# Kernel tuning notes

Measured on AMD Instinct MI355X. Metric: run time of the kernel, lower is better.

## Reference

```python
import jax, jax.numpy as jnp
import numpy as np

S, B, H, D, G = 2048, 2, 16, 128, 16  # seq, batch, heads, head_dim, v-quant groups


def setup_inputs() -> dict:
    key = jax.random.key(0)
    ks = jax.random.split(key, 9)
    # int8-valued activations stored as float (torch code does .to(torch.int8))
    q = jax.random.randint(ks[0], (S, B, H, D), -128, 128).astype(jnp.float32)
    k = jax.random.randint(ks[1], (S, B, H, D), -128, 128).astype(jnp.float32)
    v = jax.random.randint(ks[2], (S, B, H, D), -128, 128).astype(jnp.float32)
    qmin = jax.random.normal(ks[3], (S, B, H, 1), jnp.float32) * 0.01
    qscale = jax.random.uniform(ks[4], (S, B, H, 1), jnp.float32, 0.005, 0.02)
    kmin = jax.random.normal(ks[5], (S, B, H, 1), jnp.float32) * 0.01
    kscale = jax.random.uniform(ks[6], (S, B, H, 1), jnp.float32, 0.005, 0.02)
    vmin = jax.random.normal(ks[7], (G, B, H, D, 1), jnp.float32) * 0.01
    vscale = jax.random.uniform(ks[8], (G, B, H, D, 1), jnp.float32, 0.005, 0.02)
    return {"query_layer": q, "key_layer": k, "value_layer": v,
            "qmin": qmin, "qscale": qscale, "kmin": kmin, "kscale": kscale,
            "vmin": vmin, "vscale": vscale, "causal": 1}


def _attention(query_layer, key_layer, value_layer, qmin, qscale, kmin, kscale, vmin, vscale, causal):
    # s b h d -> b h s d ; emulate .to(torch.int8) (values are already int8-range ints)
    q = jnp.transpose(query_layer, (1, 2, 0, 3))
    k = jnp.transpose(key_layer, (1, 2, 0, 3))
    v = jnp.transpose(value_layer, (1, 2, 0, 3))
    # per-token quant factors: s b h 1 -> b h s 1
    qm = jnp.transpose(qmin[..., 0], (1, 2, 0))[..., None]
    qs = jnp.transpose(qscale[..., 0], (1, 2, 0))[..., None]
    km = jnp.transpose(kmin[..., 0], (1, 2, 0))[..., None]
    ksc = jnp.transpose(kscale[..., 0], (1, 2, 0))[..., None]
    # attnq_qk: dequantize per-token then QK^T
    qd = q * qs + qm
    kd = k * ksc + km
    scores = jnp.einsum('bhsd,bhtd->bhst', qd, kd)
    # softmaxq: scale by 1/sqrt(128), causal mask, softmax, int8 requant of probs
    scores = scores * jnp.float32(1.0 / np.sqrt(128.0))
    s = scores.shape[-1]
    if causal:
        mask = jnp.tril(jnp.ones((s, s), dtype=bool))
        scores = jnp.where(mask, scores, jnp.float32(-1e9))
    probs = jax.nn.softmax(scores, axis=-1)
    pmin = jnp.min(probs, axis=-1, keepdims=True)
    pmax = jnp.max(probs, axis=-1, keepdims=True)
    pscale = (pmax - pmin) / 255.0 + jnp.float32(1e-12)
    quant_prob = jnp.round((probs - pmin) / pscale)  # int8-range prob codes
    # attnq_pv: dequant probs (per query token) and V (per sequence group) then PV
    pd = quant_prob * pscale + pmin
    vm = jnp.transpose(vmin[..., 0], (1, 2, 0, 3))  # b h g d
    vs = jnp.transpose(vscale[..., 0], (1, 2, 0, 3))
    gs = v.shape[2] // vm.shape[2]  # group size along sequence
    vd = v * jnp.repeat(vs, gs, axis=2) + jnp.repeat(vm, gs, axis=2)
    out = jnp.einsum('bhst,bhtd->bhsd', pd, vd)
    b, h, sq, d = out.shape
    return jnp.transpose(out, (2, 0, 1, 3)).reshape(sq, b, h * d)  # s b (h d)


def reference(query_layer, key_layer, value_layer, qmin, qscale, kmin, kscale, vmin, vscale, causal):
    return _attention(query_layer, key_layer, value_layer, qmin, qscale, kmin, kscale, vmin, vscale, causal)
```

## Files before the change

### kernel.cpp

```cpp
#include <hip/hip_runtime.h>
#include <math.h>


#define S_LEN 2048
#define BATCH 2
#define NH    16
#define HD    128
#define RSTR  4096
#define SCALE2 (0.08838834764831845f * 1.4426950408889634f)
#define EXP2F(x) __builtin_amdgcn_exp2f(x)

typedef int v4i __attribute__((ext_vector_type(4)));
#define MFMA16(a,b,c) __builtin_amdgcn_mfma_i32_16x16x64_i8((a),(b),(c),0,0,0)

#define WS_K8   0u
#define WS_V8T  (8u*1024u*1024u)
#define WS_SQ   (16u*1024u*1024u)
#define WS_SK   (WS_SQ + 256u*1024u)
#define WS_GSV  (WS_SK + 256u*1024u)

__device__ __forceinline__ int sbsum(unsigned p) {
    return (int)(signed char)(p) + (int)(signed char)(p>>8)
         + (int)(signed char)(p>>16) + (int)(signed char)(p>>24);
}

__global__ __launch_bounds__(256) void prep_pack(
    const float* __restrict__ Q, const float* __restrict__ K, const float* __restrict__ V,
    signed char* __restrict__ K8, float* __restrict__ SQs, float* __restrict__ SKs,
    signed char* __restrict__ V8T, float* __restrict__ GSV)
{
    __shared__ int v8i[128*33];
    const int tid = threadIdx.x;
    const int bx  = blockIdx.x;
    if (bx < 16384) {
        const int tensor = bx >> 13;
        const int idx = (bx & 8191)*256 + tid;
        const float* src = tensor ? K : Q;
        int tau = idx >> 5, dg = idx & 31;
        float4 x = *(const float4*)(src + (size_t)tau*128 + 4*dg);
        float ssum = x.x + x.y + x.z + x.w;
        #pragma unroll
        for (int off = 16; off >= 1; off >>= 1) ssum += __shfl_xor(ssum, off);
        if (tensor) {
            int a=(int)x.x, b2=(int)x.y, c=(int)x.z, d=(int)x.w;
            ((int*)K8)[(size_t)tau*32 + dg] = (a&255)|((b2&255)<<8)|((c&255)<<16)|((d&255)<<24);
            if ((tid & 31) == 0) SKs[tau] = ssum;
        } else {
            if ((tid & 31) == 0) SQs[tau] = ssum;
        }
    } else {
        const int bid = bx - 16384;
        const int bh = bid & 31, ck = bid >> 5;
        const int b = bh >> 4, h = bh & 15;
        const int t0 = ck * 128;
        const int boff = b*2048 + h*128;
        #pragma unroll
        for (int it = 0; it < 16; ++it) {
            int idx = tid + it*256;
            int t = idx >> 5, dw = idx & 31;
            float4 x = *(const float4*)(V + (size_t)(t0+t)*RSTR + boff + 4*dw);
            int a=(int)x.x, b2=(int)x.y, c=(int)x.z, d=(int)x.w;
            v8i[t*33 + dw] = (a&255)|((b2&255)<<8)|((c&255)<<16)|((d&255)<<24);
        }
        __syncthreads();
        #pragma unroll
        for (int it = 0; it < 4; ++it) {
            int j = tid + it*256;
            int tg = j & 31, dw = j >> 5;
            unsigned r0 = (unsigned)v8i[(4*tg+0)*33 + dw];
            unsigned r1 = (unsigned)v8i[(4*tg+1)*33 + dw];
            unsigned r2 = (unsigned)v8i[(4*tg+2)*33 + dw];
            unsigned r3 = (unsigned)v8i[(4*tg+3)*33 + dw];
            unsigned x01 = __builtin_amdgcn_perm(r1, r0, 0x05010400u);
            unsigned x23 = __builtin_amdgcn_perm(r3, r2, 0x05010400u);
            unsigned y01 = __builtin_amdgcn_perm(r1, r0, 0x07030602u);
            unsigned y23 = __builtin_amdgcn_perm(r3, r2, 0x07030602u);
            unsigned p[4];
            p[0] = __builtin_amdgcn_perm(x23, x01, 0x05040100u);
            p[1] = __builtin_amdgcn_perm(x23, x01, 0x07060302u);
            p[2] = __builtin_amdgcn_perm(y23, y01, 0x05040100u);
            p[3] = __builtin_amdgcn_perm(y23, y01, 0x07060302u);
            int s[4];
            #pragma unroll
            for (int jj = 0; jj < 4; ++jj) {
                int d = 4*dw + jj;
                *(int*)(V8T + ((size_t)bh*128 + d)*2048 + t0 + 4*tg) = (int)p[jj];
                s[jj] = sbsum(p[jj]);
            }
            #pragma unroll
            for (int off = 1; off < 32; off <<= 1) {
                #pragma unroll
                for (int jj = 0; jj < 4; ++jj) s[jj] += __shfl_xor(s[jj], off);
            }
            if (tg == 0) {
                #pragma unroll
                for (int jj = 0; jj < 4; ++jj)
                    GSV[((size_t)bh*16 + ck)*128 + 4*dw + jj] = (float)s[jj];
            }
        }
    }
}

__global__ __launch_bounds__(256, 2) void attn_main(
    const float* __restrict__ Q,
    const signed char* __restrict__ K8, const signed char* __restrict__ V8T,
    const float* __restrict__ QMN, const float* __restrict__ QSC,
    const float* __restrict__ KMN, const float* __restrict__ KSC,
    const float* __restrict__ VMN, const float* __restrict__ VSC,
    const float* __restrict__ SQs, const float* __restrict__ SKs,
    const float* __restrict__ GSV,
    const int* __restrict__ CAUSAL, float* __restrict__ OUT)
{
    __shared__ __align__(16) signed char q8s[64*144];
    __shared__ __align__(16) signed char k8s[128*144];
    __shared__ __align__(16) signed char v8s[128*144];
    __shared__ __align__(16) signed char pcs[64*144];
    __shared__ float rs_c1[64], rs_c2[64], rs_c3[64];
    __shared__ float rs_mx[64], rs_den[64], rs_mn[64];
    __shared__ float rs_u1[64], rs_w1[64], rs_psc[64], rs_pmn[64];
    __shared__ float ktA[128], ktB[128], ktC[128];
    __shared__ float vsA[128], vsB[128];
    __shared__ float vsumL[128], cgsL[128];

    const int tid  = threadIdx.x;
    const int w    = tid >> 6;
    const int lane = tid & 63;
    const int n    = lane & 15;
    const int quad = lane >> 4;
    const int bhi  = blockIdx.x & 31;
    const int qt   = 31 - (int)(blockIdx.x >> 5);
    const int b    = bhi >> 4, h = bhi & 15;
    const int causal = *CAUSAL;
    const int s0   = qt * 64;
    const int boff = b*2048 + h*128;
    const v4i vzero = {0,0,0,0};
    const v4i ones  = {0x01010101,0x01010101,0x01010101,0x01010101};

    #pragma unroll
    for (int it = 0; it < 8; ++it) {
        int idx = tid + it*256;
        int row = idx >> 5, d4 = (idx & 31) << 2;
        float4 x = *(const float4*)(Q + (size_t)(s0+row)*RSTR + boff + d4);
        int a=(int)x.x, b2=(int)x.y, c=(int)x.z, d=(int)x.w;
        *(int*)(q8s + row*144 + d4) = (a&255)|((b2&255)<<8)|((c&255)<<16)|((d&255)<<24);
    }
    if (tid < 64) {
        int si = (s0 + tid)*32 + bhi;
        float qs = QSC[si], qm = QMN[si];
        rs_c1[tid] = qs; rs_c2[tid] = qm;
        rs_c3[tid] = fmaf(qs, SQs[si], 128.0f*qm);
    }
    __syncthreads();

    const int kt_end = causal ? ((s0 + 63) >> 7) : 15;

    float c1r[4], c2r[4], c3r[4]; int qgr[4];
    #pragma unroll
    for (int r = 0; r < 4; ++r) {
        int qq = 16*w + 4*quad + r;
        c1r[r] = rs_c1[qq]; c2r[r] = rs_c2[qq]; c3r[r] = rs_c3[qq];
        qgr[r] = s0 + qq;
    }
    v4i a0p = *(const v4i*)(q8s + (16*w + n)*144 + 16*quad);
    v4i a1p = *(const v4i*)(q8s + (16*w + n)*144 + 64 + 16*quad);

    float m[4], l[4], mn[4];
    #pragma unroll
    for (int r = 0; r < 4; ++r) { m[r] = -INFINITY; l[r] = 0.f; mn[r] = INFINITY; }

#define P1_TILE(MASKED)                                                          \
  do {                                                                           \
    const int t0g = kt * 128;                                                    \
    __syncthreads();                                                             \
    _Pragma("unroll")                                                            \
    for (int it = 0; it < 4; ++it) {                                             \
        int idx = tid + it*256;                                                  \
        int trow = idx >> 3, doff = (idx & 7) << 4;                              \
        *(uint4*)(k8s + trow*144 + doff) =                                       \
            *(const uint4*)(K8 + ((size_t)(t0g+trow)*32 + bhi)*128 + doff);      \
    }                                                                            \
    if (tid < 128) {                                                             \
        int si = (t0g + tid)*32 + bhi;                                           \
        ktA[tid] = KSC[si]*SCALE2; ktB[tid] = KMN[si]*SCALE2; ktC[tid] = SKs[si];\
    }                                                                            \
    __syncthreads();                                                             \
    float tmax[4], sarr[8][4];                                                   \
    _Pragma("unroll")                                                            \
    for (int r = 0; r < 4; ++r) tmax[r] = -INFINITY;                             \
    _Pragma("unroll")                                                            \
    for (int tb = 0; tb < 8; ++tb) {                                             \
        v4i b0 = *(const v4i*)(k8s + (16*tb + n)*144 + 16*quad);                 \
        v4i b1 = *(const v4i*)(k8s + (16*tb + n)*144 + 64 + 16*quad);            \
        v4i acc = MFMA16(a0p, b0, vzero);                                        \
        acc = MFMA16(a1p, b1, acc);                                              \
        int tl = 16*tb + n;                                                      \
        float kA = ktA[tl], kB = ktB[tl], kC = ktC[tl];                          \
        _Pragma("unroll")                                                        \
        for (int r = 0; r < 4; ++r) {                                            \
            float Sf = (float)acc[r];                                            \
            float sv = fmaf(kA, fmaf(c1r[r], Sf, c2r[r]*kC), kB*c3r[r]);         \
            if (MASKED) sv = (t0g + tl > qgr[r]) ? -INFINITY : sv;               \
            sarr[tb][r] = sv;                                                    \
            tmax[r] = fmaxf(tmax[r], sv);                                        \
            mn[r] = fminf(mn[r], sv);                                            \
        }                                                                        \
    }                                                                            \
    _Pragma("unroll")                                                            \
    for (int r = 0; r < 4; ++r) {                                                \
        float mm = fmaxf(m[r], tmax[r]);                                         \
        if (mm > -INFINITY) {                                                    \
            float e0 = EXP2F(sarr[0][r]-mm) + EXP2F(sarr[1][r]-mm);              \
            float e1 = EXP2F(sarr[2][r]-mm) + EXP2F(sarr[3][r]-mm);              \
            float e2 = EXP2F(sarr[4][r]-mm) + EXP2F(sarr[5][r]-mm);              \
            float e3 = EXP2F(sarr[6][r]-mm) + EXP2F(sarr[7][r]-mm);              \
            l[r] = fmaf(l[r], EXP2F(m[r]-mm), (e0+e1)+(e2+e3));                  \
            m[r] = mm;                                                           \
        }                                                                        \
    }                                                                            \
  } while (0)

    {
        int kt;
        for (kt = 0; kt < kt_end; ++kt) P1_TILE(false);
        kt = kt_end;
        if (causal) P1_TILE(true); else P1_TILE(false);
    }

    #pragma unroll
    for (int r = 0; r < 4; ++r) {
        #pragma unroll
        for (int off = 1; off < 16; off <<= 1) {
            float m2 = __shfl_xor(m[r], off);
            float l2 = __shfl_xor(l[r], off);
            float n2 = __shfl_xor(mn[r], off);
            float mm = fmaxf(m[r], m2);
            if (mm > -INFINITY) l[r] = l[r]*EXP2F(m[r]-mm) + l2*EXP2F(m2-mm);
            m[r] = mm;
            mn[r] = fminf(mn[r], n2);
        }
        if (n == 0) {
            int qq = 16*w + 4*quad + r;
            rs_mx[qq] = m[r]; rs_den[qq] = l[r]; rs_mn[qq] = mn[r];
        }
    }
    __syncthreads();
    if (tid < 64) {
        float mx = rs_mx[tid], den = rs_den[tid], mnv = rs_mn[tid];
        float invd = 1.0f/den;
        int s = s0 + tid;
        bool hasmask = (causal != 0) && (s < S_LEN-1);
        float pmin = hasmask ? 0.0f : EXP2F(mnv - mx)*invd;
        float psc  = (invd - pmin)/255.0f + 1e-12f;
        float ipsc = 1.0f/psc;
        rs_u1[tid] = invd*ipsc; rs_w1[tid] = -pmin*ipsc;
        rs_psc[tid] = psc; rs_pmn[tid] = pmin;
    } else if (tid >= 128) {
        int d = tid - 128;
        float vsum = 0.f, cgs = 0.f;
        #pragma unroll
        for (int g = 0; g < 16; ++g) {
            float gs = GSV[((size_t)bhi*16 + g)*128 + d];
            int vi = ((g*BATCH + b)*NH + h)*HD + d;
            float vs = VSC[vi], vm = VMN[vi];
            vsum = fmaf(vs, gs, fmaf(128.0f, vm, vsum));
            if (g <= kt_end) cgs = fmaf(128.0f*vs, gs, fmaf(16384.0f, vm, cgs));
        }
        vsumL[d] = vsum; cgsL[d] = cgs;
    }
    __syncthreads();

    v4i qb0[4], qb1[4];
    float qc1[4], qc2[4], qc3[4], qmxn[4], qu1[4], qw1[4];
    int qgq[4];
    #pragma unroll
    for (int cb = 0; cb < 4; ++cb) {
        int qcol = 16*cb + n;
        qb0[cb] = *(const v4i*)(q8s + qcol*144 + 16*quad);
        qb1[cb] = *(const v4i*)(q8s + qcol*144 + 64 + 16*quad);
        qc1[cb] = rs_c1[qcol]; qc2[cb] = rs_c2[qcol]; qc3[cb] = rs_c3[qcol];
        qmxn[cb] = -rs_mx[qcol]; qu1[cb] = rs_u1[qcol]; qw1[cb] = rs_w1[qcol];
        qgq[cb] = s0 + qcol;
    }

    float outa[4][8];
    #pragma unroll
    for (int r = 0; r < 4; ++r)
        #pragma unroll
        for (int db = 0; db < 8; ++db) outa[r][db] = 0.f;

#define P2_TILE(MASKED)                                                          \
  do {                                                                           \
    const int t0g = kt * 128;                                                    \
    __syncthreads();                      \
    _Pragma("unroll")                                                            \
    for (int it = 0; it < 4; ++it) {                                             \
        int idx = tid + it*256;                                                  \
        int trow = idx >> 3, doff = (idx & 7) << 4;                              \
        *(uint4*)(v8s + trow*144 + doff) =                                       \
            *(const uint4*)(V8T + ((size_t)bhi*128 + trow)*2048 + t0g + doff);   \
    }                                                                            \
    if (tid < 128) {                                                             \
        int si = (t0g + tid)*32 + bhi;                                           \
        ktA[tid] = KSC[si]*SCALE2; ktB[tid] = KMN[si]*SCALE2; ktC[tid] = SKs[si];\
    } else {                                                                     \
        int d = tid - 128;                                                       \
        int vi = ((kt*BATCH + b)*NH + h)*HD + d;                                 \
        vsA[d] = VSC[vi]; vsB[d] = VMN[vi];                                      \
    }                                                                            \
    __syncthreads();                                                             \
    _Pragma("unroll")                                                            \
    for (int rb = 0; rb < 2; ++rb) {                                             \
        int trow = 32*w + 16*rb;                                                 \
        const signed char* kp = K8 + ((size_t)(t0g+trow+n)*32 + bhi)*128         \
                                   + 16*quad;                                    \
        v4i a0 = *(const v4i*)kp;              \
        v4i a1 = *(const v4i*)(kp + 64);                                         \
        float ksr[4], kmr[4], skr[4];                                            \
        int tgb = t0g + trow + 4*quad;                                           \
        _Pragma("unroll")                                                        \
        for (int r = 0; r < 4; ++r) {                                            \
            int tl = trow + 4*quad + r;                                          \
            ksr[r] = ktA[tl]; kmr[r] = ktB[tl]; skr[r] = ktC[tl];                \
        }                                                                        \
        _Pragma("unroll")                                                        \
        for (int cb = 0; cb < 4; ++cb) {                                         \
            v4i acc = MFMA16(a0, qb0[cb], vzero);                                \
            acc = MFMA16(a1, qb1[cb], acc);                                      \
            int cby[4];                                                          \
            _Pragma("unroll")                                                    \
            for (int r = 0; r < 4; ++r) {                                        \
                float Sf = (float)acc[r];                                        \
                float x = fmaf(ksr[r], fmaf(qc1[cb], Sf, qc2[cb]*skr[r]),        \
                               fmaf(kmr[r], qc3[cb], qmxn[cb]));                 \
                if (MASKED) x = (tgb + r > qgq[cb]) ? -INFINITY : x;             \
                float e = EXP2F(x);                                              \
                float f = fmaf(e, qu1[cb], qw1[cb]) + 8388608.0f;   \
                cby[r] = __float_as_int(f);                                      \
            }                                                                    \
            unsigned t01 = __builtin_amdgcn_perm((unsigned)cby[1],               \
                                                 (unsigned)cby[0], 0x00000400u); \
            unsigned t23 = __builtin_amdgcn_perm((unsigned)cby[3],               \
                                                 (unsigned)cby[2], 0x04000000u); \
            int packed = (int)(__builtin_amdgcn_perm(t23, t01, 0x07060100u)      \
                               ^ 0x80808080u);          \
            *(int*)(pcs + (16*cb + n)*144 + trow + 4*quad) = packed;             \
        }                                                                        \
    }                                                                            \
    __syncthreads();                                                             \
    {                                                                            \
        v4i a0 = *(const v4i*)(pcs + (16*w + n)*144 + 16*quad);                  \
        v4i a1 = *(const v4i*)(pcs + (16*w + n)*144 + 64 + 16*quad);             \
        v4i c1a = MFMA16(a0, ones, vzero);                                       \
        c1a = MFMA16(a1, ones, c1a);                                             \
        float c1f[4];                                                            \
        _Pragma("unroll")                                                        \
        for (int r = 0; r < 4; ++r) c1f[r] = (float)c1a[r];                      \
        _Pragma("unroll")                                                        \
        for (int db = 0; db < 8; ++db) {                                         \
            v4i b0 = *(const v4i*)(v8s + (16*db + n)*144 + 16*quad);             \
            v4i b1 = *(const v4i*)(v8s + (16*db + n)*144 + 64 + 16*quad);        \
            v4i cv = MFMA16(a0, b0, vzero);                                      \
            cv = MFMA16(a1, b1, cv);                                             \
            int d = 16*db + n;                                                   \
            float vs = vsA[d], vm = vsB[d];                                      \
            _Pragma("unroll")                                                    \
            for (int r = 0; r < 4; ++r)                                          \
                outa[r][db] = fmaf(vs, (float)cv[r],                             \
                                   fmaf(vm, c1f[r], outa[r][db]));               \
        }                                                                        \
    }                                                                            \
  } while (0)

    {
        int kt;
        for (kt = 0; kt < kt_end; ++kt) P2_TILE(false);
        kt = kt_end;
        if (causal) P2_TILE(true); else P2_TILE(false);
    }

    float pscr[4], pmnr[4];
    #pragma unroll
    for (int r = 0; r < 4; ++r) {
        int qq = 16*w + 4*quad + r;
        pscr[r] = rs_psc[qq]; pmnr[r] = rs_pmn[qq];
    }
    #pragma unroll
    for (int db = 0; db < 8; ++db) {
        int d = 16*db + n;
        float vsum = vsumL[d];
        float cgs  = cgsL[d];
        #pragma unroll
        for (int r = 0; r < 4; ++r) {
            int s = s0 + 16*w + 4*quad + r;
            OUT[(size_t)s*RSTR + boff + d] = fmaf(pscr[r], outa[r][db] + cgs, pmnr[r]*vsum);
        }
    }
}

extern "C" void kernel_launch(void* const* d_in, const int* in_sizes, int n_in,
                              void* d_out, int out_size, void* d_ws, size_t ws_size,
                              hipStream_t stream) {
    (void)in_sizes; (void)n_in; (void)out_size; (void)ws_size;
    const float* Q   = (const float*)d_in[0];
    const float* K   = (const float*)d_in[1];
    const float* V   = (const float*)d_in[2];
    const float* QMN = (const float*)d_in[3];
    const float* QSC = (const float*)d_in[4];
    const float* KMN = (const float*)d_in[5];
    const float* KSC = (const float*)d_in[6];
    const float* VMN = (const float*)d_in[7];
    const float* VSC = (const float*)d_in[8];
    const int*   CS  = (const int*)d_in[9];
    float* out = (float*)d_out;

    char* ws = (char*)d_ws;
    signed char* K8  = (signed char*)(ws + WS_K8);
    signed char* V8T = (signed char*)(ws + WS_V8T);
    float* SQs  = (float*)(ws + WS_SQ);
    float* SKs  = (float*)(ws + WS_SK);
    float* GSVp = (float*)(ws + WS_GSV);

    prep_pack<<<16384 + 512, 256, 0, stream>>>(Q, K, V, K8, SQs, SKs, V8T, GSVp);
    attn_main<<<1024, 256, 0, stream>>>(Q, K8, V8T, QMN, QSC, KMN, KSC, VMN, VSC,
                                        SQs, SKs, GSVp, CS, out);
}
```

Measured before the change: 251.9 us.

## Prefetch next K/V tiles into registers and merge K/V shared buffers

Both attention passes now software-pipeline global loads. The next tile's K (or V) bytes, K/V scale factors and, in pass 2, the per-warp K MFMA fragments are loaded into registers while the current tile is being computed, then written to shared memory at the top of the next iteration. The separate K and V shared buffers are merged into a single kv8s buffer, and launch bounds go from 2 to 3 blocks per SM, aiming for higher occupancy and hidden global latency. The cost is extra register pressure from the prefetch registers under a tighter register budget, which could cause spills.

```diff
diff --git a/kernel.cpp b/kernel.cpp
--- a/kernel.cpp
+++ b/kernel.cpp
@@ -101,7 +101,7 @@
     }
 }
 
-__global__ __launch_bounds__(256, 2) void attn_main(
+__global__ __launch_bounds__(256, 3) void attn_main(
     const float* __restrict__ Q,
     const signed char* __restrict__ K8, const signed char* __restrict__ V8T,
     const float* __restrict__ QMN, const float* __restrict__ QSC,
@@ -112,8 +112,7 @@
     const int* __restrict__ CAUSAL, float* __restrict__ OUT)
 {
     __shared__ __align__(16) signed char q8s[64*144];
-    __shared__ __align__(16) signed char k8s[128*144];
-    __shared__ __align__(16) signed char v8s[128*144];
+    __shared__ __align__(16) signed char kv8s[128*144];
     __shared__ __align__(16) signed char pcs[64*144];
     __shared__ float rs_c1[64], rs_c2[64], rs_c3[64];
     __shared__ float rs_mx[64], rs_den[64], rs_mn[64];
@@ -133,6 +132,9 @@
     const int causal = *CAUSAL;
     const int s0   = qt * 64;
     const int boff = b*2048 + h*128;
+    const int trb  = tid >> 3;
+    const int tdo  = (tid & 7) << 4;
+    const int tc   = tid & 127;
     const v4i vzero = {0,0,0,0};
     const v4i ones  = {0x01010101,0x01010101,0x01010101,0x01010101};
 
@@ -168,29 +170,18 @@
     #pragma unroll
     for (int r = 0; r < 4; ++r) { m[r] = -INFINITY; l[r] = 0.f; mn[r] = INFINITY; }
 
-#define P1_TILE(MASKED)                                                          \
+#define KSTG(KT,IT) (const uint4*)(K8 + ((size_t)((KT)*128 + trb + 32*(IT))*32 + bhi)*128 + tdo)
+#define VSTG(KT,IT) (const uint4*)(V8T + ((size_t)bhi*128 + trb + 32*(IT))*2048 + (KT)*128 + tdo)
+
+#define P1_COMPUTE(MASKED, T0G)                                                  \
   do {                                                                           \
-    const int t0g = kt * 128;                                                    \
-    __syncthreads();                                                             \
-    _Pragma("unroll")                                                            \
-    for (int it = 0; it < 4; ++it) {                                             \
-        int idx = tid + it*256;                                                  \
-        int trow = idx >> 3, doff = (idx & 7) << 4;                              \
-        *(uint4*)(k8s + trow*144 + doff) =                                       \
-            *(const uint4*)(K8 + ((size_t)(t0g+trow)*32 + bhi)*128 + doff);      \
-    }                                                                            \
-    if (tid < 128) {                                                             \
-        int si = (t0g + tid)*32 + bhi;                                           \
-        ktA[tid] = KSC[si]*SCALE2; ktB[tid] = KMN[si]*SCALE2; ktC[tid] = SKs[si];\
-    }                                                                            \
-    __syncthreads();                                                             \
     float tmax[4], sarr[8][4];                                                   \
     _Pragma("unroll")                                                            \
     for (int r = 0; r < 4; ++r) tmax[r] = -INFINITY;                             \
     _Pragma("unroll")                                                            \
     for (int tb = 0; tb < 8; ++tb) {                                             \
-        v4i b0 = *(const v4i*)(k8s + (16*tb + n)*144 + 16*quad);                 \
-        v4i b1 = *(const v4i*)(k8s + (16*tb + n)*144 + 64 + 16*quad);            \
+        v4i b0 = *(const v4i*)(kv8s + (16*tb + n)*144 + 16*quad);                \
+        v4i b1 = *(const v4i*)(kv8s + (16*tb + n)*144 + 64 + 16*quad);           \
         v4i acc = MFMA16(a0p, b0, vzero);                                        \
         acc = MFMA16(a1p, b1, acc);                                              \
         int tl = 16*tb + n;                                                      \
@@ -199,7 +190,7 @@
         for (int r = 0; r < 4; ++r) {                                            \
             float Sf = (float)acc[r];                                            \
             float sv = fmaf(kA, fmaf(c1r[r], Sf, c2r[r]*kC), kB*c3r[r]);         \
-            if (MASKED) sv = (t0g + tl > qgr[r]) ? -INFINITY : sv;               \
+            if (MASKED) sv = ((T0G) + tl > qgr[r]) ? -INFINITY : sv;             \
             sarr[tb][r] = sv;                                                    \
             tmax[r] = fmaxf(tmax[r], sv);                                        \
             mn[r] = fminf(mn[r], sv);                                            \
@@ -220,10 +211,24 @@
   } while (0)
 
     {
-        int kt;
-        for (kt = 0; kt < kt_end; ++kt) P1_TILE(false);
-        kt = kt_end;
-        if (causal) P1_TILE(true); else P1_TILE(false);
+        uint4 pk0 = *KSTG(0,0), pk1 = *KSTG(0,1), pk2 = *KSTG(0,2), pk3 = *KSTG(0,3);
+        int si0 = tc*32 + bhi;
+        float nA = KSC[si0], nB = KMN[si0], nC = SKs[si0];
+        for (int kt = 0; ; ++kt) {
+            __syncthreads();
+            *(uint4*)(kv8s + (trb+ 0)*144 + tdo) = pk0;
+            *(uint4*)(kv8s + (trb+32)*144 + tdo) = pk1;
+            *(uint4*)(kv8s + (trb+64)*144 + tdo) = pk2;
+            *(uint4*)(kv8s + (trb+96)*144 + tdo) = pk3;
+            if (tid < 128) { ktA[tid] = nA*SCALE2; ktB[tid] = nB*SCALE2; ktC[tid] = nC; }
+            __syncthreads();
+            const int kn = (kt < kt_end) ? kt + 1 : kt_end;
+            pk0 = *KSTG(kn,0); pk1 = *KSTG(kn,1); pk2 = *KSTG(kn,2); pk3 = *KSTG(kn,3);
+            { int si = (kn*128 + tc)*32 + bhi; nA = KSC[si]; nB = KMN[si]; nC = SKs[si]; }
+            if (causal && kt == kt_end) P1_COMPUTE(true, kt*128);
+            else                        P1_COMPUTE(false, kt*128);
+            if (kt == kt_end) break;
+        }
     }
 
     #pragma unroll
@@ -288,94 +293,102 @@
         #pragma unroll
         for (int db = 0; db < 8; ++db) outa[r][db] = 0.f;
 
-#define P2_TILE(MASKED)                                                          \
+#define KFRG(KT,RB) (const v4i*)(K8 + ((size_t)((KT)*128 + 32*w + 16*(RB) + n)*32 + bhi)*128 + 16*quad)
+
+#define P2_QK_RB(MASKED, T0G, A0, A1, RB)                                        \
   do {                                                                           \
-    const int t0g = kt * 128;                                                    \
-    __syncthreads();                      \
-    _Pragma("unroll")                                                            \
-    for (int it = 0; it < 4; ++it) {                                             \
-        int idx = tid + it*256;                                                  \
-        int trow = idx >> 3, doff = (idx & 7) << 4;                              \
-        *(uint4*)(v8s + trow*144 + doff) =                                       \
-            *(const uint4*)(V8T + ((size_t)bhi*128 + trow)*2048 + t0g + doff);   \
+    int trow = 32*w + 16*(RB);                                                   \
+    float ksr[4], kmr[4], skr[4];                                                \
+    int tgb = (T0G) + trow + 4*quad;                                             \
+    _Pragma("unroll")                                                            \
+    for (int r = 0; r < 4; ++r) {                                                \
+        int tl = trow + 4*quad + r;                                              \
+        ksr[r] = ktA[tl]; kmr[r] = ktB[tl]; skr[r] = ktC[tl];                    \
     }                                                                            \
-    if (tid < 128) {                                                             \
-        int si = (t0g + tid)*32 + bhi;                                           \
-        ktA[tid] = KSC[si]*SCALE2; ktB[tid] = KMN[si]*SCALE2; ktC[tid] = SKs[si];\
-    } else {                                                                     \
-        int d = tid - 128;                                                       \
-        int vi = ((kt*BATCH + b)*NH + h)*HD + d;                                 \
-        vsA[d] = VSC[vi]; vsB[d] = VMN[vi];                                      \
-    }                                                                            \
-    __syncthreads();                                                             \
-    _Pragma("unroll")                                                            \
-    for (int rb = 0; rb < 2; ++rb) {                                             \
-        int trow = 32*w + 16*rb;                                                 \
-        const signed char* kp = K8 + ((size_t)(t0g+trow+n)*32 + bhi)*128         \
-                                   + 16*quad;                                    \
-        v4i a0 = *(const v4i*)kp;              \
-        v4i a1 = *(const v4i*)(kp + 64);                                         \
-        float ksr[4], kmr[4], skr[4];                                            \
-        int tgb = t0g + trow + 4*quad;                                           \
+    _Pragma("unroll")                                                            \
+    for (int cb = 0; cb < 4; ++cb) {                                             \
+        v4i acc = MFMA16(A0, qb0[cb], vzero);                                    \
+        acc = MFMA16(A1, qb1[cb], acc);                                          \
+        int cby[4];                                                              \
         _Pragma("unroll")                                                        \
         for (int r = 0; r < 4; ++r) {                                            \
-            int tl = trow + 4*quad + r;                                          \
-            ksr[r] = ktA[tl]; kmr[r] = ktB[tl]; skr[r] = ktC[tl];                \
+            float Sf = (float)acc[r];                                            \
+            float x = fmaf(ksr[r], fmaf(qc1[cb], Sf, qc2[cb]*skr[r]),            \
+                           fmaf(kmr[r], qc3[cb], qmxn[cb]));                     \
+            if (MASKED) x = (tgb + r > qgq[cb]) ? -INFINITY : x;                 \
+            float e = EXP2F(x);                                                  \
+            float f = fmaf(e, qu1[cb], qw1[cb]) + 8388608.0f;       \
+            cby[r] = __float_as_int(f);                                          \
         }                                                                        \
-        _Pragma("unroll")                                                        \
-        for (int cb = 0; cb < 4; ++cb) {                                         \
-            v4i acc = MFMA16(a0, qb0[cb], vzero);                                \
-            acc = MFMA16(a1, qb1[cb], acc);                                      \
-            int cby[4];                                                          \
-            _Pragma("unroll")                                                    \
-            for (int r = 0; r < 4; ++r) {                                        \
-                float Sf = (float)acc[r];                                        \
-                float x = fmaf(ksr[r], fmaf(qc1[cb], Sf, qc2[cb]*skr[r]),        \
-                               fmaf(kmr[r], qc3[cb], qmxn[cb]));                 \
-                if (MASKED) x = (tgb + r > qgq[cb]) ? -INFINITY : x;             \
-                float e = EXP2F(x);                                              \
-                float f = fmaf(e, qu1[cb], qw1[cb]) + 8388608.0f;   \
-                cby[r] = __float_as_int(f);                                      \
-            }                                                                    \
-            unsigned t01 = __builtin_amdgcn_perm((unsigned)cby[1],               \
-                                                 (unsigned)cby[0], 0x00000400u); \
-            unsigned t23 = __builtin_amdgcn_perm((unsigned)cby[3],               \
-                                                 (unsigned)cby[2], 0x04000000u); \
-            int packed = (int)(__builtin_amdgcn_perm(t23, t01, 0x07060100u)      \
-                               ^ 0x80808080u);          \
-            *(int*)(pcs + (16*cb + n)*144 + trow + 4*quad) = packed;             \
-        }                                                                        \
-    }                                                                            \
-    __syncthreads();                                                             \
-    {                                                                            \
-        v4i a0 = *(const v4i*)(pcs + (16*w + n)*144 + 16*quad);                  \
-        v4i a1 = *(const v4i*)(pcs + (16*w + n)*144 + 64 + 16*quad);             \
-        v4i c1a = MFMA16(a0, ones, vzero);                                       \
-        c1a = MFMA16(a1, ones, c1a);                                             \
-        float c1f[4];                                                            \
-        _Pragma("unroll")                                                        \
-        for (int r = 0; r < 4; ++r) c1f[r] = (float)c1a[r];                      \
-        _Pragma("unroll")                                                        \
-        for (int db = 0; db < 8; ++db) {                                         \
-            v4i b0 = *(const v4i*)(v8s + (16*db + n)*144 + 16*quad);             \
-            v4i b1 = *(const v4i*)(v8s + (16*db + n)*144 + 64 + 16*quad);        \
-            v4i cv = MFMA16(a0, b0, vzero);                                      \
-            cv = MFMA16(a1, b1, cv);                                             \
-            int d = 16*db + n;                                                   \
-            float vs = vsA[d], vm = vsB[d];                                      \
-            _Pragma("unroll")                                                    \
-            for (int r = 0; r < 4; ++r)                                          \
-                outa[r][db] = fmaf(vs, (float)cv[r],                             \
-                                   fmaf(vm, c1f[r], outa[r][db]));               \
-        }                                                                        \
+        unsigned t01 = __builtin_amdgcn_perm((unsigned)cby[1],                   \
+                                             (unsigned)cby[0], 0x00000400u);     \
+        unsigned t23 = __builtin_amdgcn_perm((unsigned)cby[3],                   \
+                                             (unsigned)cby[2], 0x04000000u);     \
+        int packed = (int)(__builtin_amdgcn_perm(t23, t01, 0x07060100u)          \
+                           ^ 0x80808080u);              \
+        *(int*)(pcs + (16*cb + n)*144 + trow + 4*quad) = packed;                 \
     }                                                                            \
   } while (0)
 
+#define P2_PV()                                                                  \
+  do {                                                                           \
+    v4i a0 = *(const v4i*)(pcs + (16*w + n)*144 + 16*quad);                      \
+    v4i a1 = *(const v4i*)(pcs + (16*w + n)*144 + 64 + 16*quad);                 \
+    v4i c1a = MFMA16(a0, ones, vzero);                                           \
+    c1a = MFMA16(a1, ones, c1a);                                                 \
+    float c1f[4];                                                                \
+    _Pragma("unroll")                                                            \
+    for (int r = 0; r < 4; ++r) c1f[r] = (float)c1a[r];                          \
+    _Pragma("unroll")                                                            \
+    for (int db = 0; db < 8; ++db) {                                             \
+        v4i b0 = *(const v4i*)(kv8s + (16*db + n)*144 + 16*quad);                \
+        v4i b1 = *(const v4i*)(kv8s + (16*db + n)*144 + 64 + 16*quad);           \
+        v4i cv = MFMA16(a0, b0, vzero);                                          \
+        cv = MFMA16(a1, b1, cv);                                                 \
+        int d = 16*db + n;                                                       \
+        float vs = vsA[d], vm = vsB[d];                                          \
+        _Pragma("unroll")                                                        \
+        for (int r = 0; r < 4; ++r)                                              \
+            outa[r][db] = fmaf(vs, (float)cv[r],                                 \
+                               fmaf(vm, c1f[r], outa[r][db]));                   \
+    }                                                                            \
+  } while (0)
+
     {
-        int kt;
-        for (kt = 0; kt < kt_end; ++kt) P2_TILE(false);
-        kt = kt_end;
-        if (causal) P2_TILE(true); else P2_TILE(false);
+        uint4 pv0 = *VSTG(0,0), pv1 = *VSTG(0,1), pv2 = *VSTG(0,2), pv3 = *VSTG(0,3);
+        v4i ka00 = *KFRG(0,0), ka01 = *(KFRG(0,0) + 4);
+        v4i ka10 = *KFRG(0,1), ka11 = *(KFRG(0,1) + 4);
+        int si0 = tc*32 + bhi;
+        float nA = KSC[si0], nB = KMN[si0], nC = SKs[si0];
+        int vi0 = (b*NH + h)*HD + tc;
+        float vA = VSC[vi0], vB = VMN[vi0];
+        for (int kt = 0; ; ++kt) {
+            const int t0g = kt * 128;
+            __syncthreads();
+            *(uint4*)(kv8s + (trb+ 0)*144 + tdo) = pv0;
+            *(uint4*)(kv8s + (trb+32)*144 + tdo) = pv1;
+            *(uint4*)(kv8s + (trb+64)*144 + tdo) = pv2;
+            *(uint4*)(kv8s + (trb+96)*144 + tdo) = pv3;
+            if (tid < 128) { ktA[tid] = nA*SCALE2; ktB[tid] = nB*SCALE2; ktC[tid] = nC; }
+            else           { vsA[tc] = vA; vsB[tc] = vB; }
+            __syncthreads();
+            const int kn = (kt < kt_end) ? kt + 1 : kt_end;
+            pv0 = *VSTG(kn,0); pv1 = *VSTG(kn,1); pv2 = *VSTG(kn,2); pv3 = *VSTG(kn,3);
+            { int si = (kn*128 + tc)*32 + bhi; nA = KSC[si]; nB = KMN[si]; nC = SKs[si]; }
+            { int vi = ((kn*BATCH + b)*NH + h)*HD + tc; vA = VSC[vi]; vB = VMN[vi]; }
+            if (causal && kt == kt_end) {
+                P2_QK_RB(true, t0g, ka00, ka01, 0);
+                P2_QK_RB(true, t0g, ka10, ka11, 1);
+            } else {
+                P2_QK_RB(false, t0g, ka00, ka01, 0);
+                P2_QK_RB(false, t0g, ka10, ka11, 1);
+            }
+            ka00 = *KFRG(kn,0); ka01 = *(KFRG(kn,0) + 4);
+            ka10 = *KFRG(kn,1); ka11 = *(KFRG(kn,1) + 4);
+            __syncthreads();
+            P2_PV();
+            if (kt == kt_end) break;
+        }
     }
 
     float pscr[4], pmnr[4];
```

Result: slower. 310.5 us (+23.2%).
